# Kernel optimization log

Hardware: AMD Instinct MI355X
Metric: run time of the kernel (lower is better)

## Reference

```python
import jax, jax.numpy as jnp
import numpy as np

N = 10000      # nodes
E = 160000     # edges
G = 128        # graphs in batch
DIMS = [16, 32, 32]  # in_channels, then conv output dims
HID = 25       # edge-MLP hidden width
EPS = 1e-5     # batch-norm eps


def setup_inputs() -> dict:
    key = jax.random.key(0)
    ks = iter(jax.random.split(key, 40))
    inp = {}
    inp["x"] = jax.random.normal(next(ks), (N, DIMS[0]), dtype=jnp.float32)
    inp["edge_attr"] = jax.random.uniform(next(ks), (E, 3), dtype=jnp.float32)
    inp["edge_index"] = jax.random.randint(next(ks), (2, E), 0, N, dtype=jnp.int32)
    inp["batch"] = jnp.sort(jax.random.randint(next(ks), (N,), 0, G, dtype=jnp.int32))
    for i in range(2):
        din, dout = DIMS[i], DIMS[i + 1]
        inp[f"w1_{i}"] = jax.random.normal(next(ks), (3, HID), dtype=jnp.float32) * 0.3
        inp[f"b1_{i}"] = jnp.zeros((HID,), jnp.float32)
        inp[f"g_{i}"] = jnp.ones((HID,), jnp.float32)
        inp[f"be_{i}"] = jnp.zeros((HID,), jnp.float32)
        inp[f"w2_{i}"] = jax.random.normal(next(ks), (HID, din * dout), dtype=jnp.float32) * 0.05
        inp[f"b2_{i}"] = jnp.zeros((din * dout,), jnp.float32)
        inp[f"wr_{i}"] = jax.random.normal(next(ks), (din, dout), dtype=jnp.float32) * 0.1
        inp[f"bc_{i}"] = jnp.zeros((dout,), jnp.float32)
    inp["wfc"] = jax.random.normal(next(ks), (DIMS[-1], 1), dtype=jnp.float32) * 0.1
    inp["bfc"] = jnp.zeros((1,), jnp.float32)
    return inp


def _ecn(x, edge_attr, layers, wfc, bfc, edge_index, batch):
    src, dst = edge_index[0], edge_index[1]
    deg = jax.ops.segment_sum(jnp.ones((E,), x.dtype), dst, num_segments=N)
    deg = jnp.clip(deg, 1.0)[:, None]          # [N,1], PyG mean clamps count>=1
    for (w1, b1, g, be, w2, b2, wr, bc) in layers:
        # edge MLP: Linear(3,25) -> BatchNorm(batch stats) -> ReLU -> Linear(25, in*out)
        h = edge_attr @ w1 + b1                 # [E,25]
        mu = h.mean(axis=0)
        var = h.var(axis=0)
        h = (h - mu) * jax.lax.rsqrt(var + EPS) * g + be
        h = jax.nn.relu(h)
        w = (h @ w2 + b2).reshape(E, x.shape[1], -1)   # [E,in,out] per-edge weights
        msg = jnp.einsum('ei,eio->eo', x[src], w)      # gather + per-edge matmul
        agg = jax.ops.segment_sum(msg, dst, num_segments=N) / deg  # scatter-mean
        x = agg + x @ wr + bc                   # root transform + bias
        x = jax.nn.elu(x)
    # global mean pool over graphs
    gsum = jax.ops.segment_sum(x, batch, num_segments=G)
    gcnt = jnp.clip(jax.ops.segment_sum(jnp.ones((N,), x.dtype), batch, num_segments=G), 1.0)
    pooled = gsum / gcnt[:, None]               # [G, dims[-1]]
    return pooled @ wfc + bfc                   # fc MLP last layer is plain Linear


def reference(x, edge_attr, edge_index, batch,
              w1_0, b1_0, g_0, be_0, w2_0, b2_0, wr_0, bc_0,
              w1_1, b1_1, g_1, be_1, w2_1, b2_1, wr_1, bc_1,
              wfc, bfc):
    layers = [
        (w1_0, b1_0, g_0, be_0, w2_0, b2_0, wr_0, bc_0),
        (w1_1, b1_1, g_1, be_1, w2_1, b2_1, wr_1, bc_1),
    ]
    return _ecn(x, edge_attr, layers, wfc, bfc, edge_index, batch)
```

## Files before the change

### kernel.cpp

```cpp
#include <hip/hip_runtime.h>
#include <math.h>

#define NN   10000
#define EE   160000
#define GG   128
#define HIDK 25
#define KROWS 32
#define DOUT 32
#define EPSBN 1e-5f

#define OFF_CUR   0
#define OFF_GSUM  10016
#define OFF_DEGC  14112
#define ZERO_FLOATS 24128
#define OFF_MOP   24128
#define OFF_W1F0  25664
#define OFF_B1F0  25744
#define OFF_W1F1  25776
#define OFF_B1F1  25856
#define OFF_ROW   25888
#define OFF_SRC   35904
#define OFF_EA    195904
#define OFF_WB0   835904
#define OFF_WB1   852288
#define OFF_X1    885056
#define TOTAL_FLOATS 1205056

__device__ inline float wave_red(float v) {
    for (int off = 32; off; off >>= 1) v += __shfl_down(v, off);
    return v;
}

__global__ void k_momdeg(const float* __restrict__ ea, const int* __restrict__ ei,
                         float* __restrict__ mop, int* __restrict__ degc) {
    __shared__ float ls[4][9];
    float s[9];
#pragma unroll
    for (int j = 0; j < 9; j++) s[j] = 0.f;
    int t = threadIdx.x;
    for (int e = blockIdx.x * 256 + t; e < EE; e += 128 * 256) {
        float a0 = ea[3 * e], a1 = ea[3 * e + 1], a2 = ea[3 * e + 2];
        s[0] += a0; s[1] += a1; s[2] += a2;
        s[3] += a0 * a0; s[4] += a0 * a1; s[5] += a0 * a2;
        s[6] += a1 * a1; s[7] += a1 * a2; s[8] += a2 * a2;
        atomicAdd(degc + ei[EE + e], 1);
    }
    int w = t >> 6, lane = t & 63;
#pragma unroll
    for (int j = 0; j < 9; j++) {
        float r = wave_red(s[j]);
        if (lane == 0) ls[w][j] = r;
    }
    __syncthreads();
    if (t < 9) mop[blockIdx.x * 12 + t] = ls[0][t] + ls[1][t] + ls[2][t] + ls[3][t];
}

template <int DIN>
__device__ inline void wpack(int idx, const float* __restrict__ w2,
                             const float* __restrict__ b2, float* __restrict__ wbig) {
    int k = idx / (DIN * DOUT);
    int rem = idx - k * (DIN * DOUT);
    int i4 = rem / (4 * DOUT);
    int rem2 = rem - i4 * (4 * DOUT);
    int o = rem2 >> 2, c = rem2 & 3;
    int i = i4 * 4 + c;
    float v = 0.f;
    if (k < HIDK) v = w2[(k * DIN + i) * DOUT + o];
    else if (k == HIDK) v = b2[i * DOUT + o];
    wbig[idx] = v;
}

__global__ void k_prep(const int* __restrict__ degc, int* __restrict__ row_start,
                       const float* __restrict__ mop,
                       const float* __restrict__ w1_0, const float* __restrict__ b1_0,
                       const float* __restrict__ g_0, const float* __restrict__ be_0,
                       const float* __restrict__ w1_1, const float* __restrict__ b1_1,
                       const float* __restrict__ g_1, const float* __restrict__ be_1,
                       float* __restrict__ w1f0, float* __restrict__ b1f0,
                       float* __restrict__ w1f1, float* __restrict__ b1f1,
                       const float* __restrict__ w2_0, const float* __restrict__ b2_0,
                       const float* __restrict__ w2_1, const float* __restrict__ b2_1,
                       float* __restrict__ wb0, float* __restrict__ wb1) {
    int b = blockIdx.x, t = threadIdx.x;
    if (b == 0) {
        __shared__ int p[256];
        const int CHUNK = 40;
        int base = t * CHUNK;
        int sum = 0;
        if (t < 250) {
            for (int i = 0; i < CHUNK; i++) sum += degc[base + i];
        }
        p[t] = sum;
        __syncthreads();
        for (int off = 1; off < 256; off <<= 1) {
            int v = (t >= off) ? p[t - off] : 0;
            __syncthreads();
            p[t] += v;
            __syncthreads();
        }
        int excl = p[t] - sum;
        if (t < 250) {
            int run = excl;
            for (int i = 0; i < CHUNK; i++) {
                row_start[base + i] = run;
                run += degc[base + i];
            }
        }
        if (t == 0) row_start[NN] = EE;
    } else if (b == 1) {
        __shared__ float mo[9];
        if (t < 9) {
            float s = 0.f;
            for (int bb = 0; bb < 128; bb++) s += mop[bb * 12 + t];
            mo[t] = s;
        }
        __syncthreads();
        int grp = t >> 5, j = t & 31;
        if (grp < 2 && j < HIDK) {
            const float* w1 = grp ? w1_1 : w1_0;
            const float* b1 = grp ? b1_1 : b1_0;
            const float* g  = grp ? g_1  : g_0;
            const float* be = grp ? be_1 : be_0;
            float* w1f = grp ? w1f1 : w1f0;
            float* b1f = grp ? b1f1 : b1f0;
            const float inv = 1.0f / (float)EE;
            float m0 = mo[0] * inv, m1 = mo[1] * inv, m2 = mo[2] * inv;
            float c00 = mo[3] * inv - m0 * m0, c01 = mo[4] * inv - m0 * m1, c02 = mo[5] * inv - m0 * m2;
            float c11 = mo[6] * inv - m1 * m1, c12 = mo[7] * inv - m1 * m2, c22 = mo[8] * inv - m2 * m2;
            float w0 = w1[j], wa = w1[25 + j], wb = w1[50 + j];
            float mean = m0 * w0 + m1 * wa + m2 * wb + b1[j];
            float var = w0 * w0 * c00 + wa * wa * c11 + wb * wb * c22
                      + 2.f * (w0 * wa * c01 + w0 * wb * c02 + wa * wb * c12);
            float sc = g[j] * rsqrtf(var + EPSBN);
            w1f[j] = w0 * sc; w1f[25 + j] = wa * sc; w1f[50 + j] = wb * sc;
            b1f[j] = (b1[j] - mean) * sc + be[j];
        }
    } else {
        int idx = (b - 2) * 256 + t;
        if (idx < KROWS * 16 * DOUT) wpack<16>(idx, w2_0, b2_0, wb0);
        else if (idx < KROWS * 16 * DOUT + KROWS * 32 * DOUT)
            wpack<32>(idx - KROWS * 16 * DOUT, w2_1, b2_1, wb1);
    }
}

__global__ void k_scatter(const int* __restrict__ ei, const float* __restrict__ ea,
                          const int* __restrict__ row_start,
                          int* __restrict__ cur, int* __restrict__ csr_src,
                          float* __restrict__ eacsr) {
    int e = blockIdx.x * blockDim.x + threadIdx.x;
    if (e >= EE) return;
    int d = ei[EE + e];
    int pos = atomicAdd(cur + d, 1);
    int idx = row_start[d] + pos;
    csr_src[idx] = ei[e];
    float4 av = { ea[3 * e], ea[3 * e + 1], ea[3 * e + 2], 0.f };
    *(float4*)(eacsr + 4 * (size_t)idx) = av;
}

template <int DIN, int KPL, bool FINAL>
__global__ __launch_bounds__(256, 4)
void k_fused(const int* __restrict__ row_start,
             const int* __restrict__ csr_src,
             const float* __restrict__ eacsr,
             const float* __restrict__ w1f, const float* __restrict__ b1f,
             const float* __restrict__ wbig, const float* __restrict__ xin,
             const float* __restrict__ wr, const float* __restrict__ bc,
             const int* __restrict__ batch,
             float* __restrict__ xout, float* __restrict__ gsum) {
    __shared__ __align__(16) float Slds[4][KROWS][DIN];
    __shared__ float Olds[4][DOUT];
    __shared__ __align__(16) float hb[4][2][32];
    int t = threadIdx.x;
    int w = t >> 6, lane = t & 63;
    int ln = w >> 1, q = w & 1;
    int n = blockIdx.x * 2 + ln;
    int start = row_start[n], end = row_start[n + 1];

    int il = lane & (DIN - 1);
    int kh = lane / DIN;
    int kme = lane & 31;
    int half = lane >> 5;

    float c0 = 0.f, c1 = 0.f, c2 = 0.f, c3 = 0.f;
    if (kme < HIDK) {
        c0 = w1f[kme]; c1 = w1f[25 + kme]; c2 = w1f[50 + kme]; c3 = b1f[kme];
    } else if (kme == HIDK) {
        c3 = 1.0f;
    }

    float s[KPL];
#pragma unroll
    for (int j = 0; j < KPL; j++) s[j] = 0.f;

    const float4* ea4 = (const float4*)eacsr;

    int p = start + q;
    int sA = 0, sB = 0, vB = 0, qBs = 0;
    if (p < end) {
        int qB = p + 2; vB = (qB < end); qBs = vB ? qB : p;
        sA = csr_src[p];
        sB = csr_src[qBs];
    }
    while (p < end) {
        float4 av = ea4[half ? qBs : p];
        float xA = xin[sA * DIN + il];
        float xB = xin[sB * DIN + il];
        if (!vB) xB = 0.f;
        int pn = p + 4;
        int sAn = 0, sBn = 0, vBn = 0, qBsn = 0;
        if (pn < end) {
            int qBn = pn + 2; vBn = (qBn < end); qBsn = vBn ? qBn : pn;
            sAn = csr_src[pn];
            sBn = csr_src[qBsn];
        }
        float hv = av.x * c0 + av.y * c1 + av.z * c2 + c3;
        hv = hv > 0.f ? hv : 0.f;
        hb[w][half][kme] = hv;
        const float4* hA4 = (const float4*)&hb[w][0][kh * KPL];
        const float4* hB4 = (const float4*)&hb[w][1][kh * KPL];
#pragma unroll
        for (int j4 = 0; j4 < KPL / 4; j4++) {
            float4 ha = hA4[j4];
            s[j4 * 4 + 0] += ha.x * xA; s[j4 * 4 + 1] += ha.y * xA;
            s[j4 * 4 + 2] += ha.z * xA; s[j4 * 4 + 3] += ha.w * xA;
        }
#pragma unroll
        for (int j4 = 0; j4 < KPL / 4; j4++) {
            float4 hbv = hB4[j4];
            s[j4 * 4 + 0] += hbv.x * xB; s[j4 * 4 + 1] += hbv.y * xB;
            s[j4 * 4 + 2] += hbv.z * xB; s[j4 * 4 + 3] += hbv.w * xB;
        }
        p = pn; sA = sAn; sB = sBn; vB = vBn; qBs = qBsn;
    }
#pragma unroll
    for (int j = 0; j < KPL; j++)
        Slds[w][kh * KPL + j][il] = s[j];
    __syncthreads();

    constexpr int PER = KROWS * DIN / 4;
    for (int f = t; f < 2 * PER; f += 256) {
        int node = f / PER, rem = f - node * PER;
        float4* dst = (float4*)&Slds[2 * node][0][0];
        const float4* sp = (const float4*)&Slds[2 * node + 1][0][0];
        float4 a = dst[rem], b = sp[rem];
        a.x += b.x; a.y += b.y; a.z += b.z; a.w += b.w;
        dst[rem] = a;
    }
    __syncthreads();

    int o = lane & 31, hf = lane >> 5;
    const float4* wb4 = (const float4*)wbig;
    float acc0 = 0.f, acc1 = 0.f;
    int kbase = q * (KROWS / 2) + hf * (KROWS / 4);
#pragma unroll
    for (int kk = 0; kk < KROWS / 4; kk++) {
        int k = kbase + kk;
        float a = 0.f;
#pragma unroll
        for (int i4 = 0; i4 < DIN / 4; i4++) {
            float4 sv = *(const float4*)&Slds[2 * ln][k][i4 * 4];
            float4 wv = wb4[(k * (DIN / 4) + i4) * 32 + o];
            a += sv.x * wv.x + sv.y * wv.y + sv.z * wv.z + sv.w * wv.w;
        }
        if (kk & 1) acc1 += a; else acc0 += a;
    }
    float acc = acc0 + acc1;
    acc += __shfl_xor(acc, 32);
    if (hf == 0) Olds[w][o] = acc;
    __syncthreads();

    if (t < 64) {
        int ln2 = t >> 5, o2 = t & 31;
        int n2 = blockIdx.x * 2 + ln2;
        int cnt2 = row_start[n2 + 1] - row_start[n2];
        float d = (float)cnt2; if (d < 1.f) d = 1.f;
        float r = (Olds[2 * ln2][o2] + Olds[2 * ln2 + 1][o2]) / d + bc[o2];
#pragma unroll
        for (int i = 0; i < DIN; i++) r += xin[n2 * DIN + i] * wr[i * DOUT + o2];
        r = r > 0.f ? r : expm1f(r);
        if (FINAL) atomicAdd(gsum + batch[n2] * DOUT + o2, r);
        else xout[n2 * DOUT + o2] = r;
    }
}

__global__ void k_fc(const float* __restrict__ gsum, const int* __restrict__ batch,
                     const float* __restrict__ wfc, const float* __restrict__ bfc,
                     float* __restrict__ out) {
    int g = threadIdx.x;
    if (g >= GG) return;
    int lo = 0, hi = NN;
    while (lo < hi) { int mid = (lo + hi) >> 1; if (batch[mid] < g) lo = mid + 1; else hi = mid; }
    int lb = lo;
    lo = 0; hi = NN;
    while (lo < hi) { int mid = (lo + hi) >> 1; if (batch[mid] < g + 1) lo = mid + 1; else hi = mid; }
    float c = (float)(lo - lb); if (c < 1.f) c = 1.f;
    float acc = 0.f;
#pragma unroll
    for (int o = 0; o < DOUT; o++) acc += gsum[g * DOUT + o] * wfc[o];
    out[g] = acc / c + bfc[0];
}

extern "C" void kernel_launch(void* const* d_in, const int* in_sizes, int n_in,
                              void* d_out, int out_size, void* d_ws, size_t ws_size,
                              hipStream_t stream) {
    const float* x     = (const float*)d_in[0];
    const float* ea    = (const float*)d_in[1];
    const int*   ei    = (const int*)d_in[2];
    const int*   batch = (const int*)d_in[3];
    const float* w1_0 = (const float*)d_in[4];
    const float* b1_0 = (const float*)d_in[5];
    const float* g_0  = (const float*)d_in[6];
    const float* be_0 = (const float*)d_in[7];
    const float* w2_0 = (const float*)d_in[8];
    const float* b2_0 = (const float*)d_in[9];
    const float* wr_0 = (const float*)d_in[10];
    const float* bc_0 = (const float*)d_in[11];
    const float* w1_1 = (const float*)d_in[12];
    const float* b1_1 = (const float*)d_in[13];
    const float* g_1  = (const float*)d_in[14];
    const float* be_1 = (const float*)d_in[15];
    const float* w2_1 = (const float*)d_in[16];
    const float* b2_1 = (const float*)d_in[17];
    const float* wr_1 = (const float*)d_in[18];
    const float* bc_1 = (const float*)d_in[19];
    const float* wfc  = (const float*)d_in[20];
    const float* bfc  = (const float*)d_in[21];

    float* ws    = (float*)d_ws;
    int*   cur   = (int*)(ws + OFF_CUR);
    float* gsum  = ws + OFF_GSUM;
    int*   degc  = (int*)(ws + OFF_DEGC);
    float* mop   = ws + OFF_MOP;
    float* w1f0  = ws + OFF_W1F0;
    float* b1f0  = ws + OFF_B1F0;
    float* w1f1  = ws + OFF_W1F1;
    float* b1f1  = ws + OFF_B1F1;
    int*   row   = (int*)(ws + OFF_ROW);
    int*   csrc  = (int*)(ws + OFF_SRC);
    float* eacsr = ws + OFF_EA;
    float* wb0   = ws + OFF_WB0;
    float* wb1   = ws + OFF_WB1;
    float* x1    = ws + OFF_X1;

    hipMemsetAsync(ws, 0, (size_t)ZERO_FLOATS * sizeof(float), stream);

    k_momdeg<<<128, 256, 0, stream>>>(ea, ei, mop, degc);
    k_prep<<<194, 256, 0, stream>>>(degc, row, mop,
                                    w1_0, b1_0, g_0, be_0, w1_1, b1_1, g_1, be_1,
                                    w1f0, b1f0, w1f1, b1f1,
                                    w2_0, b2_0, w2_1, b2_1, wb0, wb1);
    k_scatter<<<(EE + 255) / 256, 256, 0, stream>>>(ei, ea, row, cur, csrc, eacsr);

    k_fused<16, 8, false><<<NN / 2, 256, 0, stream>>>(row, csrc, eacsr, w1f0, b1f0,
                                                      wb0, x, wr_0, bc_0, batch, x1, gsum);
    k_fused<32, 16, true><<<NN / 2, 256, 0, stream>>>(row, csrc, eacsr, w1f1, b1f1,
                                                      wb1, x1, wr_1, bc_1, batch, nullptr, gsum);

    k_fc<<<1, 128, 0, stream>>>(gsum, batch, wfc, bfc, (float*)d_out);
}
```

Measured before the change: 223.0 us.

## Software-pipeline edge loop with double-buffered LDS and share weight loads across nodes

Rewrites the per-edge accumulation loop as a two-stage software pipeline: edge attributes and source indices are prefetched two iterations ahead, x values one ahead, and the hidden activations go into a double-buffered LDS slot so the next edge's hidden vector is computed while the current one is consumed. The K-reduction epilogue is reorganised so each wave handles a slice of K rows for both nodes in the block, loading each weight float4 once and using it for two nodes, with the four partial sums combined at the end. Launch bounds are raised to 8 blocks per CU to seek more occupancy. This adds register pressure, which the tighter launch bound may turn into spills.

```diff
diff --git a/kernel.cpp b/kernel.cpp
--- a/kernel.cpp
+++ b/kernel.cpp
@@ -158,7 +158,7 @@
 }
 
 template <int DIN, int KPL, bool FINAL>
-__global__ __launch_bounds__(256, 4)
+__global__ __launch_bounds__(256, 8)
 void k_fused(const int* __restrict__ row_start,
              const int* __restrict__ csr_src,
              const float* __restrict__ eacsr,
@@ -168,8 +168,8 @@
              const int* __restrict__ batch,
              float* __restrict__ xout, float* __restrict__ gsum) {
     __shared__ __align__(16) float Slds[4][KROWS][DIN];
-    __shared__ float Olds[4][DOUT];
-    __shared__ __align__(16) float hb[4][2][32];
+    __shared__ float Olds[2][4][DOUT];
+    __shared__ __align__(16) float hb[4][2][2][32];
     int t = threadIdx.x;
     int w = t >> 6, lane = t & 63;
     int ln = w >> 1, q = w & 1;
@@ -195,42 +195,66 @@
     const float4* ea4 = (const float4*)eacsr;
 
     int p = start + q;
-    int sA = 0, sB = 0, vB = 0, qBs = 0;
+    int sA0 = 0, sB0 = 0, vB0 = 0;
+    int sA1 = 0, sB1 = 0, vB1 = 0;
+    float xA = 0.f, xB = 0.f;
+    float4 av1 = {0.f, 0.f, 0.f, 0.f};
+    int buf = 0;
+
     if (p < end) {
-        int qB = p + 2; vB = (qB < end); qBs = vB ? qB : p;
-        sA = csr_src[p];
-        sB = csr_src[qBs];
+        int qB = p + 2; vB0 = (qB < end); int qBs0 = vB0 ? qB : p;
+        sA0 = csr_src[p]; sB0 = csr_src[qBs0];
+        int p1 = p + 4;
+        int qBs1 = 0;
+        if (p1 < end) {
+            int qB1 = p1 + 2; vB1 = (qB1 < end); qBs1 = vB1 ? qB1 : p1;
+            sA1 = csr_src[p1]; sB1 = csr_src[qBs1];
+        }
+        float4 av0 = ea4[half ? qBs0 : p];
+        xA = xin[sA0 * DIN + il];
+        xB = xin[sB0 * DIN + il];
+        if (p1 < end) av1 = ea4[half ? qBs1 : p1];
+        float hv = av0.x * c0 + av0.y * c1 + av0.z * c2 + c3;
+        hv = hv > 0.f ? hv : 0.f;
+        hb[w][0][half][kme] = hv;
     }
     while (p < end) {
-        float4 av = ea4[half ? qBs : p];
-        float xA = xin[sA * DIN + il];
-        float xB = xin[sB * DIN + il];
-        if (!vB) xB = 0.f;
-        int pn = p + 4;
-        int sAn = 0, sBn = 0, vBn = 0, qBsn = 0;
-        if (pn < end) {
-            int qBn = pn + 2; vBn = (qBn < end); qBsn = vBn ? qBn : pn;
-            sAn = csr_src[pn];
-            sBn = csr_src[qBsn];
-        }
-        float hv = av.x * c0 + av.y * c1 + av.z * c2 + c3;
-        hv = hv > 0.f ? hv : 0.f;
-        hb[w][half][kme] = hv;
-        const float4* hA4 = (const float4*)&hb[w][0][kh * KPL];
-        const float4* hB4 = (const float4*)&hb[w][1][kh * KPL];
+        int p1 = p + 4, p2 = p + 8;
+        int sA2 = 0, sB2 = 0, vB2 = 0;
+        float4 av2 = {0.f, 0.f, 0.f, 0.f};
+        if (p2 < end) {
+            int qB2 = p2 + 2; vB2 = (qB2 < end); int qBs2 = vB2 ? qB2 : p2;
+            sA2 = csr_src[p2]; sB2 = csr_src[qBs2];
+            av2 = ea4[half ? qBs2 : p2];
+        }
+        float xAn = 0.f, xBn = 0.f;
+        if (p1 < end) { xAn = xin[sA1 * DIN + il]; xBn = xin[sB1 * DIN + il]; }
+        const float4* hA4 = (const float4*)&hb[w][buf][0][kh * KPL];
+        const float4* hB4 = (const float4*)&hb[w][buf][1][kh * KPL];
+        float4 ha[KPL / 4], hbv[KPL / 4];
+#pragma unroll
+        for (int j4 = 0; j4 < KPL / 4; j4++) { ha[j4] = hA4[j4]; hbv[j4] = hB4[j4]; }
+        if (p1 < end) {
+            float hv = av1.x * c0 + av1.y * c1 + av1.z * c2 + c3;
+            hv = hv > 0.f ? hv : 0.f;
+            hb[w][buf ^ 1][half][kme] = hv;
+        }
+        float xBm = vB0 ? xB : 0.f;
 #pragma unroll
         for (int j4 = 0; j4 < KPL / 4; j4++) {
-            float4 ha = hA4[j4];
-            s[j4 * 4 + 0] += ha.x * xA; s[j4 * 4 + 1] += ha.y * xA;
-            s[j4 * 4 + 2] += ha.z * xA; s[j4 * 4 + 3] += ha.w * xA;
+            s[j4 * 4 + 0] += ha[j4].x * xA; s[j4 * 4 + 1] += ha[j4].y * xA;
+            s[j4 * 4 + 2] += ha[j4].z * xA; s[j4 * 4 + 3] += ha[j4].w * xA;
         }
 #pragma unroll
         for (int j4 = 0; j4 < KPL / 4; j4++) {
-            float4 hbv = hB4[j4];
-            s[j4 * 4 + 0] += hbv.x * xB; s[j4 * 4 + 1] += hbv.y * xB;
-            s[j4 * 4 + 2] += hbv.z * xB; s[j4 * 4 + 3] += hbv.w * xB;
-        }
-        p = pn; sA = sAn; sB = sBn; vB = vBn; qBs = qBsn;
+            s[j4 * 4 + 0] += hbv[j4].x * xBm; s[j4 * 4 + 1] += hbv[j4].y * xBm;
+            s[j4 * 4 + 2] += hbv[j4].z * xBm; s[j4 * 4 + 3] += hbv[j4].w * xBm;
+        }
+        p = p1;
+        sA0 = sA1; sB0 = sB1; vB0 = vB1;
+        sA1 = sA2; sB1 = sB2; vB1 = vB2;
+        xA = xAn; xB = xBn; av1 = av2;
+        buf ^= 1;
     }
 #pragma unroll
     for (int j = 0; j < KPL; j++)
@@ -248,25 +272,29 @@
     }
     __syncthreads();
 
-    int o = lane & 31, hf = lane >> 5;
-    const float4* wb4 = (const float4*)wbig;
-    float acc0 = 0.f, acc1 = 0.f;
-    int kbase = q * (KROWS / 2) + hf * (KROWS / 4);
-#pragma unroll
-    for (int kk = 0; kk < KROWS / 4; kk++) {
-        int k = kbase + kk;
-        float a = 0.f;
-#pragma unroll
-        for (int i4 = 0; i4 < DIN / 4; i4++) {
-            float4 sv = *(const float4*)&Slds[2 * ln][k][i4 * 4];
-            float4 wv = wb4[(k * (DIN / 4) + i4) * 32 + o];
-            a += sv.x * wv.x + sv.y * wv.y + sv.z * wv.z + sv.w * wv.w;
-        }
-        if (kk & 1) acc1 += a; else acc0 += a;
-    }
-    float acc = acc0 + acc1;
-    acc += __shfl_xor(acc, 32);
-    if (hf == 0) Olds[w][o] = acc;
+    {
+        int o = lane & 31, hf = lane >> 5;
+        constexpr int I4H = DIN / 8;
+        const float4* wb4 = (const float4*)wbig;
+        float acc0 = 0.f, acc1 = 0.f;
+        int kbase = w * (KROWS / 4);
+#pragma unroll
+        for (int kk = 0; kk < KROWS / 4; kk++) {
+            int k = kbase + kk;
+#pragma unroll
+            for (int j = 0; j < I4H; j++) {
+                int i4 = hf * I4H + j;
+                float4 wv = wb4[(k * (DIN / 4) + i4) * 32 + o];
+                float4 s0 = *(const float4*)&Slds[0][k][i4 * 4];
+                float4 s1 = *(const float4*)&Slds[2][k][i4 * 4];
+                acc0 += s0.x * wv.x + s0.y * wv.y + s0.z * wv.z + s0.w * wv.w;
+                acc1 += s1.x * wv.x + s1.y * wv.y + s1.z * wv.z + s1.w * wv.w;
+            }
+        }
+        acc0 += __shfl_xor(acc0, 32);
+        acc1 += __shfl_xor(acc1, 32);
+        if (hf == 0) { Olds[0][w][o] = acc0; Olds[1][w][o] = acc1; }
+    }
     __syncthreads();
 
     if (t < 64) {
@@ -274,7 +302,9 @@
         int n2 = blockIdx.x * 2 + ln2;
         int cnt2 = row_start[n2 + 1] - row_start[n2];
         float d = (float)cnt2; if (d < 1.f) d = 1.f;
-        float r = (Olds[2 * ln2][o2] + Olds[2 * ln2 + 1][o2]) / d + bc[o2];
+        float agg = Olds[ln2][0][o2] + Olds[ln2][1][o2]
+                  + Olds[ln2][2][o2] + Olds[ln2][3][o2];
+        float r = agg / d + bc[o2];
 #pragma unroll
         for (int i = 0; i < DIN; i++) r += xin[n2 * DIN + i] * wr[i * DOUT + o2];
         r = r > 0.f ? r : expm1f(r);
```

Result: slower. 253.9 us (+13.9%).
